# Kernel tuning notes

Hardware: AMD Instinct MI355X
Metric: run time of the kernel (lower is better)

The kernel has to match this reference:

```python
import jax, jax.numpy as jnp
import numpy as np

IN_FEATURES = 4096
OUT_FEATURES = 4096
TOKENS = 8192
QMAX = 127.0


def setup_inputs() -> dict:
    key = jax.random.key(0)
    k1, k2, k3, k4 = jax.random.split(key, 4)
    x = jax.random.normal(k1, (TOKENS, IN_FEATURES), dtype=jnp.float32)
    # int8 quantized weights in [-127, 127]
    Wq = jax.random.randint(k2, (OUT_FEATURES, IN_FEATURES), -127, 128, dtype=jnp.int32).astype(jnp.int8)
    # per-row absmax scales (positive)
    row_scales = jax.random.uniform(k3, (OUT_FEATURES,), dtype=jnp.float32, minval=0.01, maxval=1.0)
    bias_param = jax.random.normal(k4, (OUT_FEATURES,), dtype=jnp.float32)
    return {"x": x, "Wq": Wq, "row_scales": row_scales, "bias_param": bias_param}


def reference(x, Wq, row_scales, bias_param):
    # rowwise dequant: W[o, i] = Wq[o, i] * row_scales[o] / 127
    W_dequant = Wq.astype(x.dtype) * (row_scales.astype(x.dtype) / QMAX)[:, None]  # [O, I]
    Y = jnp.matmul(x, W_dequant.T)  # [T, O]
    return Y + bias_param.astype(x.dtype)
```

## Files before the change

### kernel.cpp

```cpp
#include <hip/hip_runtime.h>

#define M_TOK 8192
#define N_OUT 4096
#define K_IN  4096

#define AS1 __attribute__((address_space(1)))
#define AS3 __attribute__((address_space(3)))

typedef __attribute__((ext_vector_type(4))) int i32x4;
typedef __attribute__((ext_vector_type(16))) int i32x16;

template <int OFF>
__device__ __forceinline__ i32x4 dsri(unsigned addr) {
    i32x4 r;
    asm volatile("ds_read_b128 %0, %1 offset:%2" : "=v"(r) : "v"(addr), "n"(OFF));
    return r;
}


__global__ __launch_bounds__(256) void quant_x_kernel(
    const float* __restrict__ x, signed char* __restrict__ xq,
    float* __restrict__ tok_scale)
{
    const int row = blockIdx.x;
    const float4* xr = reinterpret_cast<const float4*>(x + (size_t)row * K_IN);
    const int t = threadIdx.x;
    float4 v[4];
    float m = 0.f;
#pragma unroll
    for (int i = 0; i < 4; ++i) {
        v[i] = xr[t + 256 * i];
        m = fmaxf(m, fmaxf(fmaxf(fabsf(v[i].x), fabsf(v[i].y)),
                           fmaxf(fabsf(v[i].z), fabsf(v[i].w))));
    }
#pragma unroll
    for (int off = 32; off >= 1; off >>= 1)
        m = fmaxf(m, __shfl_xor(m, off, 64));
    __shared__ float wmax[4];
    if ((t & 63) == 0) wmax[t >> 6] = m;
    __syncthreads();
    m = fmaxf(fmaxf(wmax[0], wmax[1]), fmaxf(wmax[2], wmax[3]));
    if (t == 0) tok_scale[row] = m * (1.0f / 127.0f);
    const float inv = (m > 0.f) ? (127.0f / m) : 0.f;
    int* xqi = reinterpret_cast<int*>(xq + (size_t)row * K_IN);
#pragma unroll
    for (int i = 0; i < 4; ++i) {
        const int q0 = __float2int_rn(v[i].x * inv) & 255;
        const int q1 = __float2int_rn(v[i].y * inv) & 255;
        const int q2 = __float2int_rn(v[i].z * inv) & 255;
        const int q3 = __float2int_rn(v[i].w * inv) & 255;
        xqi[t + 256 * i] = q0 | (q1 << 8) | (q2 << 16) | (q3 << 24);
    }
}


__global__ __launch_bounds__(256) void retile_x_kernel(
    const signed char* __restrict__ xq8, signed char* __restrict__ xqF)
{
    __shared__ __align__(16) char lds[32768];
    const int t = threadIdx.x;
    const int rb = blockIdx.x >> 2;
    const int kc = blockIdx.x & 3;

    const size_t srcBase = (size_t)rb * 32 * K_IN + (size_t)kc * 1024;
#pragma unroll
    for (int j = 0; j < 8; ++j) {
        const int u = j * 256 + t;
        const int row = u >> 6, gc = u & 63;
        const i32x4 v = *reinterpret_cast<const i32x4*>(
            xq8 + srcBase + (size_t)row * K_IN + gc * 16);
        *reinterpret_cast<i32x4*>(
            lds + ((row * 64 + (gc ^ (row & 7))) * 16)) = v;
    }
    __syncthreads();

    const int l = t & 63;
    const int W = t >> 6;
    const int row = l & 31;
    const int hi = l >> 5;
    i32x4* dst0 = reinterpret_cast<i32x4*>(xqF) +
                  ((size_t)rb * 128 + kc * 32) * 64 + l;
#pragma unroll
    for (int i = 0; i < 8; ++i) {
        const int kfl = W * 8 + i;
        const int gc = (kfl * 2 + hi) ^ (row & 7);
        const i32x4 v = *reinterpret_cast<const i32x4*>(
            lds + ((row * 64 + gc) * 16));
        dst0[(size_t)kfl * 64] = v;
    }
}


__global__ __launch_bounds__(256) void pack_w_frag_kernel(
    const int* __restrict__ wq, signed char* __restrict__ wqF)
{
    const int t = threadIdx.x;
    const int l = t & 63;
    const int W = t >> 6;
    const int rb = blockIdx.x >> 3;
    const int pc = blockIdx.x & 7;
    const int r = rb * 32 + (l & 31);
    const int4* wr4 = reinterpret_cast<const int4*>(wq) + (size_t)r * 1024;
    i32x4* outF = reinterpret_cast<i32x4*>(wqF) + (size_t)rb * 128 * 64 + l;
#pragma unroll
    for (int q = 0; q < 4; ++q) {
        const int f = W + 4 * (pc * 4 + q);
        const int c4 = f * 8 + (l >> 5) * 4;
        i32x4 o;
#pragma unroll
        for (int j = 0; j < 4; ++j) {
            const int4 a = wr4[c4 + j];
            o[j] = (a.x & 255) | ((a.y & 255) << 8) | ((a.z & 255) << 16) | ((a.w & 255) << 24);
        }
        outF[(size_t)f * 64] = o;
    }
}


#define BKB 64
#define NKT (K_IN / BKB)
#define SLOT 32768
#define NSLOT 4

#define MFMA(a, b, c) c = __builtin_amdgcn_mfma_i32_32x32x32_i8(a, b, c, 0, 0, 0)

#define RD12(P, aB, bB)                        \
    P##_A0 = dsri<0>(aB);                      \
    P##_A1 = dsri<2048>(aB);                   \
    P##_A2 = dsri<4096>(aB);                   \
    P##_A3 = dsri<6144>(aB);                   \
    P##_B0 = dsri<0>(bB);                      \
    P##_B1 = dsri<2048>(bB);                   \
    P##_A4 = dsri<1024>(aB);                   \
    P##_A5 = dsri<3072>(aB);                   \
    P##_A6 = dsri<5120>(aB);                   \
    P##_A7 = dsri<7168>(aB);                   \
    P##_B2 = dsri<1024>(bB);                   \
    P##_B3 = dsri<3072>(bB);

#define CL8_0(P)                                              \
    MFMA(P##_A0, P##_B0, acc00); MFMA(P##_A0, P##_B1, acc01); \
    MFMA(P##_A1, P##_B0, acc10); MFMA(P##_A1, P##_B1, acc11); \
    MFMA(P##_A2, P##_B0, acc20); MFMA(P##_A2, P##_B1, acc21); \
    MFMA(P##_A3, P##_B0, acc30); MFMA(P##_A3, P##_B1, acc31);

#define CL8_1(P)                                              \
    MFMA(P##_A4, P##_B2, acc00); MFMA(P##_A4, P##_B3, acc01); \
    MFMA(P##_A5, P##_B2, acc10); MFMA(P##_A5, P##_B3, acc11); \
    MFMA(P##_A6, P##_B2, acc20); MFMA(P##_A6, P##_B3, acc21); \
    MFMA(P##_A7, P##_B2, acc30); MFMA(P##_A7, P##_B3, acc31);

#define GBODY(T, C, N, DO_STAGE)                                          \
    {                                                                     \
        asm volatile("s_waitcnt lgkmcnt(6)" ::: "memory");                \
        __builtin_amdgcn_sched_barrier(0);                                \
        __builtin_amdgcn_s_setprio(1);                                    \
        CL8_0(C)                                                          \
        __builtin_amdgcn_s_setprio(0);                                    \
        __builtin_amdgcn_sched_barrier(0);                                \
        const unsigned aN_ = aBase + (unsigned)((((T) + 1) & 3) * SLOT);  \
        const unsigned bN_ = bBase + (unsigned)((((T) + 1) & 3) * SLOT);  \
        RD12(N, aN_, bN_)                                                 \
        if (DO_STAGE) stageAB((T) + 3);                                   \
        asm volatile("s_waitcnt lgkmcnt(12)" ::: "memory");               \
        __builtin_amdgcn_sched_barrier(0);                                \
        __builtin_amdgcn_s_setprio(1);                                    \
        CL8_1(C)                                                          \
        __builtin_amdgcn_s_setprio(0);                                    \
        __builtin_amdgcn_sched_barrier(0);                                \
        if (DO_STAGE) { asm volatile("s_waitcnt vmcnt(4)" ::: "memory"); }\
        else          { asm volatile("s_waitcnt vmcnt(0)" ::: "memory"); }\
        __builtin_amdgcn_sched_barrier(0);                                \
        __builtin_amdgcn_s_barrier();                                     \
        __builtin_amdgcn_sched_barrier(0);                                \
    }

#define GFINAL(C)                                                         \
    {                                                                     \
        asm volatile("s_waitcnt lgkmcnt(6)" ::: "memory");                \
        __builtin_amdgcn_sched_barrier(0);                                \
        __builtin_amdgcn_s_setprio(1);                                    \
        CL8_0(C)                                                          \
        __builtin_amdgcn_s_setprio(0);                                    \
        asm volatile("s_waitcnt lgkmcnt(0)" ::: "memory");                \
        __builtin_amdgcn_sched_barrier(0);                                \
        __builtin_amdgcn_s_setprio(1);                                    \
        CL8_1(C)                                                          \
        __builtin_amdgcn_s_setprio(0);                                    \
        __builtin_amdgcn_sched_barrier(0);                                \
    }

__global__ __launch_bounds__(512, 2) void qgemm_i8f_kernel(
    const signed char* __restrict__ xqF,
    const signed char* __restrict__ wqF,
    const float* __restrict__ tok_scale,
    const float* __restrict__ row_scales,
    const float* __restrict__ bias,
    float* __restrict__ out)
{
    __shared__ __align__(16) char smem[NSLOT * SLOT + 1024];

    const int tid = threadIdx.x;
    const int l = tid & 63;
    const int w = tid >> 6;
    const int wr = w >> 2;
    const int wc = w & 3;

    const int bid = blockIdx.x;
    const int swz = (bid & 7) * 64 + (bid >> 3);
    const int bm = swz >> 4;
    const int bn = swz & 15;

    const signed char* aS = xqF + ((size_t)(bm * 8 + w) * 128) * 1024 + (size_t)l * 16;
    const signed char* bS = wqF + ((size_t)(bn * 8 + w) * 128) * 1024 + (size_t)l * 16;
    char* aDst = smem + w * 2048;
    char* bDst = smem + 16384 + w * 2048;

    auto stageAB = [&](int tt) {
        const int sb = (tt & 3) * SLOT;
        const signed char* a0 = aS + (size_t)tt * 2048;
        const signed char* b0 = bS + (size_t)tt * 2048;
        __builtin_amdgcn_global_load_lds((const AS1 void*)a0,          (AS3 void*)(aDst + sb),        16, 0, 0);
        __builtin_amdgcn_global_load_lds((const AS1 void*)(a0 + 1024), (AS3 void*)(aDst + sb + 1024), 16, 0, 0);
        __builtin_amdgcn_global_load_lds((const AS1 void*)b0,          (AS3 void*)(bDst + sb),        16, 0, 0);
        __builtin_amdgcn_global_load_lds((const AS1 void*)(b0 + 1024), (AS3 void*)(bDst + sb + 1024), 16, 0, 0);
    };

    const unsigned sbase = (unsigned)(uintptr_t)(AS3 char*)smem;
    const unsigned aBase = sbase + (unsigned)(wr * 8192 + l * 16);
    const unsigned bBase = sbase + 16384u + (unsigned)(wc * 4096 + l * 16);

    i32x16 acc00 = {0}, acc01 = {0}, acc10 = {0}, acc11 = {0};
    i32x16 acc20 = {0}, acc21 = {0}, acc30 = {0}, acc31 = {0};

    i32x4 X_A0, X_A1, X_A2, X_A3, X_A4, X_A5, X_A6, X_A7, X_B0, X_B1, X_B2, X_B3;
    i32x4 Y_A0, Y_A1, Y_A2, Y_A3, Y_A4, Y_A5, Y_A6, Y_A7, Y_B0, Y_B1, Y_B2, Y_B3;

    stageAB(0); stageAB(1); stageAB(2);
    asm volatile("s_waitcnt vmcnt(4)" ::: "memory");
    __builtin_amdgcn_sched_barrier(0);
    __builtin_amdgcn_s_barrier();
    __builtin_amdgcn_sched_barrier(0);
    RD12(X, aBase, bBase)

    for (int t = 0; t < 62; t += 2) {
        GBODY(t,     X, Y, (t + 3 < NKT));
        GBODY(t + 1, Y, X, (t + 4 < NKT));
    }
    GBODY(62, X, Y, false);
    GFINAL(Y)

    float* ts = (float*)(smem + NSLOT * SLOT);
    if (tid < 256) ts[tid] = tok_scale[bm * 256 + tid];
    __syncthreads();

    const int cl = l & 31;
    const int rg4 = (l >> 5) * 4;
    const int gcol0 = bn * 256 + wc * 64;
    float cs[2], bb[2];
#pragma unroll
    for (int nb = 0; nb < 2; ++nb) {
        const int col = gcol0 + nb * 32 + cl;
        cs[nb] = row_scales[col] * (1.0f / 127.0f);
        bb[nb] = bias[col];
    }
    const i32x16* accs[4][2] = {{&acc00, &acc01}, {&acc10, &acc11},
                                {&acc20, &acc21}, {&acc30, &acc31}};
#pragma unroll
    for (int mb = 0; mb < 4; ++mb) {
#pragma unroll
        for (int reg = 0; reg < 16; ++reg) {
            const int rloc = wr * 128 + mb * 32 + (reg & 3) + 8 * (reg >> 2) + rg4;
            const float tsv = ts[rloc];
            float* orow = out + (size_t)(bm * 256 + rloc) * N_OUT + gcol0 + cl;
#pragma unroll
            for (int nb = 0; nb < 2; ++nb) {
                const int a = (*accs[mb][nb])[reg];
                orow[nb * 32] = (float)a * tsv * cs[nb] + bb[nb];
            }
        }
    }
}


extern "C" void kernel_launch(void* const* d_in, const int* in_sizes, int n_in,
                              void* d_out, int out_size, void* d_ws, size_t ws_size,
                              hipStream_t stream) {
    const float* x = (const float*)d_in[0];
    const int* wq = (const int*)d_in[1];
    const float* row_scales = (const float*)d_in[2];
    const float* bias = (const float*)d_in[3];
    float* out = (float*)d_out;

    signed char* xq8 = (signed char*)d_ws;
    signed char* xqF = xq8 + (size_t)M_TOK * K_IN;
    signed char* wqF = xqF + (size_t)M_TOK * K_IN;
    float* tok_scale = (float*)(wqF + (size_t)N_OUT * K_IN);
    (void)ws_size;

    quant_x_kernel<<<M_TOK, 256, 0, stream>>>(x, xq8, tok_scale);
    pack_w_frag_kernel<<<1024, 256, 0, stream>>>(wq, wqF);
    retile_x_kernel<<<1024, 256, 0, stream>>>(xq8, xqF);

    const int nblocks = (M_TOK / 256) * (N_OUT / 256);
    qgemm_i8f_kernel<<<nblocks, 512, 0, stream>>>(
        xqF, wqF, tok_scale, row_scales, bias, out);
}
```

Before: 192.1 us.

## Load B operand fragments directly from global into registers, bypassing LDS

The int8 GEMM no longer stages the weight (B) tiles through shared memory. Each wave now reads its pre-packed B fragments straight from global memory into registers, one k-step ahead, while only the activation (A) tiles still go through the 4-slot LDS ring. This halves the LDS slot size and removes the B-side LDS writes and reads. In exchange, global-load latency for B sits on the critical path with only one step of prefetch, and waves that share a column tile issue duplicate global reads of B.

```diff
diff --git a/kernel.cpp b/kernel.cpp
--- a/kernel.cpp
+++ b/kernel.cpp
@@ -119,24 +119,26 @@
 
 #define BKB 64
 #define NKT (K_IN / BKB)
-#define SLOT 32768
+#define SLOT 16384
 #define NSLOT 4
 
 #define MFMA(a, b, c) c = __builtin_amdgcn_mfma_i32_32x32x32_i8(a, b, c, 0, 0, 0)
 
-#define RD12(P, aB, bB)                        \
+#define RD8(P, aB)                             \
     P##_A0 = dsri<0>(aB);                      \
     P##_A1 = dsri<2048>(aB);                   \
     P##_A2 = dsri<4096>(aB);                   \
     P##_A3 = dsri<6144>(aB);                   \
-    P##_B0 = dsri<0>(bB);                      \
-    P##_B1 = dsri<2048>(bB);                   \
     P##_A4 = dsri<1024>(aB);                   \
     P##_A5 = dsri<3072>(aB);                   \
     P##_A6 = dsri<5120>(aB);                   \
-    P##_A7 = dsri<7168>(aB);                   \
-    P##_B2 = dsri<1024>(bB);                   \
-    P##_B3 = dsri<3072>(bB);
+    P##_A7 = dsri<7168>(aB);
+
+#define RDB(P, TT)                                             \
+    P##_B0 = bSrc[(size_t)((TT) * 2 + 0) * 64];                \
+    P##_B1 = bSrc[(size_t)(128 + (TT) * 2 + 0) * 64];          \
+    P##_B2 = bSrc[(size_t)((TT) * 2 + 1) * 64];                \
+    P##_B3 = bSrc[(size_t)(128 + (TT) * 2 + 1) * 64];
 
 #define CL8_0(P)                                              \
     MFMA(P##_A0, P##_B0, acc00); MFMA(P##_A0, P##_B1, acc01); \
@@ -152,24 +154,23 @@
 
 #define GBODY(T, C, N, DO_STAGE)                                          \
     {                                                                     \
-        asm volatile("s_waitcnt lgkmcnt(6)" ::: "memory");                \
+        asm volatile("s_waitcnt lgkmcnt(4)" ::: "memory");                \
         __builtin_amdgcn_sched_barrier(0);                                \
         __builtin_amdgcn_s_setprio(1);                                    \
         CL8_0(C)                                                          \
         __builtin_amdgcn_s_setprio(0);                                    \
         __builtin_amdgcn_sched_barrier(0);                                \
         const unsigned aN_ = aBase + (unsigned)((((T) + 1) & 3) * SLOT);  \
-        const unsigned bN_ = bBase + (unsigned)((((T) + 1) & 3) * SLOT);  \
-        RD12(N, aN_, bN_)                                                 \
-        if (DO_STAGE) stageAB((T) + 3);                                   \
-        asm volatile("s_waitcnt lgkmcnt(12)" ::: "memory");               \
+        RD8(N, aN_)                                                       \
+        RDB(N, (T) + 1)                                                   \
+        if (DO_STAGE) stageA((T) + 3);                                    \
+        asm volatile("s_waitcnt lgkmcnt(8)" ::: "memory");                \
         __builtin_amdgcn_sched_barrier(0);                                \
         __builtin_amdgcn_s_setprio(1);                                    \
         CL8_1(C)                                                          \
         __builtin_amdgcn_s_setprio(0);                                    \
         __builtin_amdgcn_sched_barrier(0);                                \
-        if (DO_STAGE) { asm volatile("s_waitcnt vmcnt(4)" ::: "memory"); }\
-        else          { asm volatile("s_waitcnt vmcnt(0)" ::: "memory"); }\
+        asm volatile("s_waitcnt vmcnt(2)" ::: "memory");                  \
         __builtin_amdgcn_sched_barrier(0);                                \
         __builtin_amdgcn_s_barrier();                                     \
         __builtin_amdgcn_sched_barrier(0);                                \
@@ -177,7 +178,7 @@
 
 #define GFINAL(C)                                                         \
     {                                                                     \
-        asm volatile("s_waitcnt lgkmcnt(6)" ::: "memory");                \
+        asm volatile("s_waitcnt lgkmcnt(4)" ::: "memory");                \
         __builtin_amdgcn_sched_barrier(0);                                \
         __builtin_amdgcn_s_setprio(1);                                    \
         CL8_0(C)                                                          \
@@ -190,7 +191,7 @@
         __builtin_amdgcn_sched_barrier(0);                                \
     }
 
-__global__ __launch_bounds__(512, 2) void qgemm_i8f_kernel(
+__global__ __launch_bounds__(512, 2) void qgemm_i8b_kernel(
     const signed char* __restrict__ xqF,
     const signed char* __restrict__ wqF,
     const float* __restrict__ tok_scale,
@@ -212,23 +213,20 @@
     const int bn = swz & 15;
 
     const signed char* aS = xqF + ((size_t)(bm * 8 + w) * 128) * 1024 + (size_t)l * 16;
-    const signed char* bS = wqF + ((size_t)(bn * 8 + w) * 128) * 1024 + (size_t)l * 16;
     char* aDst = smem + w * 2048;
-    char* bDst = smem + 16384 + w * 2048;
-
-    auto stageAB = [&](int tt) {
+
+    auto stageA = [&](int tt) {
         const int sb = (tt & 3) * SLOT;
         const signed char* a0 = aS + (size_t)tt * 2048;
-        const signed char* b0 = bS + (size_t)tt * 2048;
         __builtin_amdgcn_global_load_lds((const AS1 void*)a0,          (AS3 void*)(aDst + sb),        16, 0, 0);
         __builtin_amdgcn_global_load_lds((const AS1 void*)(a0 + 1024), (AS3 void*)(aDst + sb + 1024), 16, 0, 0);
-        __builtin_amdgcn_global_load_lds((const AS1 void*)b0,          (AS3 void*)(bDst + sb),        16, 0, 0);
-        __builtin_amdgcn_global_load_lds((const AS1 void*)(b0 + 1024), (AS3 void*)(bDst + sb + 1024), 16, 0, 0);
     };
+
+    const i32x4* bSrc = reinterpret_cast<const i32x4*>(
+        wqF + ((size_t)(bn * 8 + wc * 2) * 128) * 1024) + l;
 
     const unsigned sbase = (unsigned)(uintptr_t)(AS3 char*)smem;
     const unsigned aBase = sbase + (unsigned)(wr * 8192 + l * 16);
-    const unsigned bBase = sbase + 16384u + (unsigned)(wc * 4096 + l * 16);
 
     i32x16 acc00 = {0}, acc01 = {0}, acc10 = {0}, acc11 = {0};
     i32x16 acc20 = {0}, acc21 = {0}, acc30 = {0}, acc31 = {0};
@@ -236,12 +234,13 @@
     i32x4 X_A0, X_A1, X_A2, X_A3, X_A4, X_A5, X_A6, X_A7, X_B0, X_B1, X_B2, X_B3;
     i32x4 Y_A0, Y_A1, Y_A2, Y_A3, Y_A4, Y_A5, Y_A6, Y_A7, Y_B0, Y_B1, Y_B2, Y_B3;
 
-    stageAB(0); stageAB(1); stageAB(2);
+    RDB(X, 0)
+    stageA(0); stageA(1); stageA(2);
     asm volatile("s_waitcnt vmcnt(4)" ::: "memory");
     __builtin_amdgcn_sched_barrier(0);
     __builtin_amdgcn_s_barrier();
     __builtin_amdgcn_sched_barrier(0);
-    RD12(X, aBase, bBase)
+    RD8(X, aBase)
 
     for (int t = 0; t < 62; t += 2) {
         GBODY(t,     X, Y, (t + 3 < NKT));
@@ -303,6 +302,6 @@
     retile_x_kernel<<<1024, 256, 0, stream>>>(xq8, xqF);
 
     const int nblocks = (M_TOK / 256) * (N_OUT / 256);
-    qgemm_i8f_kernel<<<nblocks, 512, 0, stream>>>(
+    qgemm_i8b_kernel<<<nblocks, 512, 0, stream>>>(
         xqF, wqF, tok_scale, row_scales, bias, out);
 }
```

Measured after the change: 204.7 us. 6.6% more time.
